# Performance work log

Measured on AMD Instinct MI355X. Metric: run time of the kernel, lower is better.

The kernel has to match this reference:

```python
import jax, jax.numpy as jnp
import numpy as np

H, W = 256, 256
DX, DY = 1.0, 1.0
EI, KC, GC = 1.0, 1.0, 1.0
LAYERS = [2, 256, 512, 1024, H * W]
B = 64


def _d2x(f, dx):
    # reflect-pad width 1 on x (last axis), stencil [1, -2, 1]
    p = jnp.pad(f, ((0, 0), (0, 0), (0, 0), (1, 1)), mode='reflect')
    return (p[..., :-2] - 2.0 * p[..., 1:-1] + p[..., 2:]) / (dx * dx)


def _d2y(f, dy):
    p = jnp.pad(f, ((0, 0), (0, 0), (1, 1), (0, 0)), mode='reflect')
    return (p[:, :, :-2, :] - 2.0 * p[:, :, 1:-1, :] + p[:, :, 2:, :]) / (dy * dy)


def setup_inputs() -> dict:
    key = jax.random.key(0)
    ks = jax.random.split(key, 10)
    inp = {
        'x_coloc': jax.random.normal(ks[0], (B, LAYERS[0]), jnp.float32),
        'P': jax.random.normal(ks[1], (B, H * W), jnp.float32),
    }
    for i in range(4):
        inp[f'W{i + 1}'] = jax.random.normal(ks[2 + i], (LAYERS[i], LAYERS[i + 1]), jnp.float32) / np.sqrt(LAYERS[i]).astype(np.float32)
        inp[f'b{i + 1}'] = jnp.zeros((LAYERS[i + 1],), jnp.float32)
    return inp


def reference(x_coloc, P, W1, b1, W2, b2, W3, b3, W4, b4):
    # MLP field predictor: Linear+ReLU x3, final Linear -> [B, H*W]
    h = jax.nn.relu(x_coloc @ W1 + b1)
    h = jax.nn.relu(h @ W2 + b2)
    h = jax.nn.relu(h @ W3 + b3)
    f = h @ W4 + b4                      # [B, H*W]
    fm = f.reshape(B, 1, H, W)

    fx2 = _d2x(fm, DX)                   # d2/dx2
    fy2 = _d2y(fm, DY)                   # d2/dy2
    lap = fx2 + fy2
    biharmonic = _d2x(lap, DX) + _d2y(lap, DY)

    residual = EI * biharmonic + GC * (fx2 + fy2) + KC * fm - P.reshape(B, 1, H, W)
    return residual.reshape(B, H * W)
```

## Files before the change

kernel.cpp:

```cpp
#include <hip/hip_runtime.h>
#include <hip/hip_bf16.h>


#define BATCH 64
#define NPIX 65536

typedef __attribute__((ext_vector_type(8))) short short8_t;
typedef __attribute__((ext_vector_type(4))) float f32x4;

__device__ __forceinline__ short f2bf(float x) {
    __hip_bfloat16 h = __float2bfloat16(x);
    short s;
    __builtin_memcpy(&s, &h, 2);
    return s;
}

__global__ void k_layer12(const float* __restrict__ x, const float* __restrict__ W1,
                          const float* __restrict__ b1, const float* __restrict__ W2,
                          const float* __restrict__ b2, short* __restrict__ h2b) {
    __shared__ float As[16][64];
    __shared__ float Ws[64][16];
    int tid = threadIdx.x;
    int tn = tid & 15, tm = tid >> 4;
    int n0 = blockIdx.x * 16, m0 = blockIdx.y * 16;
    float acc = 0.f;
    for (int k0 = 0; k0 < 256; k0 += 64) {
#pragma unroll
        for (int j = 0; j < 4; ++j) {
            int e = j * 256 + tid;
            int m = m0 + (e >> 6), kk = k0 + (e & 63);
            float v = x[m * 2 + 0] * W1[kk] + x[m * 2 + 1] * W1[256 + kk] + b1[kk];
            As[e >> 6][e & 63] = v > 0.f ? v : 0.f;
        }
#pragma unroll
        for (int j = 0; j < 4; ++j) {
            int e = j * 256 + tid;
            Ws[e >> 4][e & 15] = W2[(k0 + (e >> 4)) * 512 + n0 + (e & 15)];
        }
        __syncthreads();
#pragma unroll
        for (int k = 0; k < 64; ++k)
            acc += As[tm][k] * Ws[k][tn];
        __syncthreads();
    }
    acc += b2[n0 + tn];
    acc = acc > 0.f ? acc : 0.f;
    h2b[(m0 + tm) * 512 + n0 + tn] = f2bf(acc);
}

__global__ __launch_bounds__(64) void k_layer3(
        const short* __restrict__ A,
        const float* __restrict__ W3,
        const float* __restrict__ b3,
        short* __restrict__ h3b) {
    __shared__ float Wt[2][32 * 16];
    const int lane = threadIdx.x;
    const int lr = lane & 15;
    const int g = lane >> 4;
    const int n0 = blockIdx.x * 16;

    f32x4 acc[4];
#pragma unroll
    for (int a = 0; a < 4; ++a) acc[a] = {0.f, 0.f, 0.f, 0.f};

    const short* ap = A + lr * 512 + g * 8;

    auto stage = [&](int b, int s) {
#pragma unroll
        for (int i = 0; i < 2; ++i) {
            int c = i * 64 + lane;
            int k = c >> 2, q = c & 3;
            const float* src = W3 + (size_t)(s * 32 + k) * 1024 + n0 + q * 4;
            __builtin_amdgcn_global_load_lds(
                (const __attribute__((address_space(1))) void*)src,
                (__attribute__((address_space(3))) void*)((char*)&Wt[b][0] + c * 16),
                16, 0, 0);
        }
    };

    short8_t aC[4], aN[4];
    stage(0, 0);
#pragma unroll
    for (int mt = 0; mt < 4; ++mt)
        aC[mt] = *(const short8_t*)(ap + mt * 8192);

    for (int s = 0; s < 16; ++s) {
        const int cur = s & 1;
        if (s < 15) {
            stage(cur ^ 1, s + 1);
#pragma unroll
            for (int mt = 0; mt < 4; ++mt)
                aN[mt] = *(const short8_t*)(ap + mt * 8192 + (s + 1) * 32);
            asm volatile("s_waitcnt vmcnt(6)" ::: "memory");
        } else {
            asm volatile("s_waitcnt vmcnt(0)" ::: "memory");
        }
        __builtin_amdgcn_sched_barrier(0);

        short8_t bfr;
#pragma unroll
        for (int j = 0; j < 8; ++j)
            bfr[j] = f2bf(Wt[cur][(g * 8 + j) * 16 + lr]);
#pragma unroll
        for (int mt = 0; mt < 4; ++mt)
            acc[mt] = __builtin_amdgcn_mfma_f32_16x16x32_bf16(aC[mt], bfr, acc[mt], 0, 0, 0);

        if (s < 15) {
#pragma unroll
            for (int mt = 0; mt < 4; ++mt) aC[mt] = aN[mt];
        }
    }

    float bb = b3[n0 + lr];
#pragma unroll
    for (int mt = 0; mt < 4; ++mt) {
        int rowb = mt * 16 + g * 4;
#pragma unroll
        for (int r = 0; r < 4; ++r) {
            float v = acc[mt][r] + bb;
            v = v > 0.f ? v : 0.f;
            h3b[(rowb + r) * 1024 + n0 + lr] = f2bf(v);
        }
    }
}

__global__ __launch_bounds__(256) void k_gemm_mfma(
        const short* __restrict__ A,
        const float* __restrict__ W,
        const float* __restrict__ bias,
        float* __restrict__ f) {
    __shared__ float Wt[2][32 * 128];
    __shared__ short At[2][4 * 64 * 8];
    const int tid = threadIdx.x;
    const int w = tid >> 6;
    const int lane = tid & 63;
    const int lr = lane & 15;
    const int g = lane >> 4;
    const int n0 = blockIdx.x * 128;

    f32x4 acc[4][2];
#pragma unroll
    for (int a = 0; a < 4; ++a)
#pragma unroll
        for (int b = 0; b < 2; ++b)
            acc[a][b] = {0.f, 0.f, 0.f, 0.f};

    auto stage = [&](int b, int s) {
#pragma unroll
        for (int i = 0; i < 4; ++i) {
            int c = i * 256 + tid;
            int k = c >> 5;
            int q4 = (c & 31) * 4;
            int csw = q4 ^ (((k >> 3) & 1) << 4);
            const float* src = W + (size_t)(s * 32 + k) * NPIX + n0 + csw;
            __builtin_amdgcn_global_load_lds(
                (const __attribute__((address_space(1))) void*)src,
                (__attribute__((address_space(3))) void*)((char*)&Wt[b][0] + c * 16),
                16, 0, 0);
        }
        {
            int kq = tid >> 6;
            int ms = tid & 63;
            int md = ms ^ (kq << 2);
            const short* asrc = A + md * 1024 + s * 32 + kq * 8;
            __builtin_amdgcn_global_load_lds(
                (const __attribute__((address_space(1))) void*)asrc,
                (__attribute__((address_space(3))) void*)((char*)&At[b][0] + tid * 16),
                16, 0, 0);
        }
    };

    stage(0, 0);

    for (int s = 0; s < 32; ++s) {
        const int cur = s & 1;
        if (s < 31) {
            stage(cur ^ 1, s + 1);
            asm volatile("s_waitcnt vmcnt(5)" ::: "memory");
        } else {
            asm volatile("s_waitcnt vmcnt(0)" ::: "memory");
        }
        __builtin_amdgcn_sched_barrier(0);
        __builtin_amdgcn_s_barrier();
        __builtin_amdgcn_sched_barrier(0);

        short8_t afr[4];
#pragma unroll
        for (int mt = 0; mt < 4; ++mt) {
            int mrow = mt * 16 + lr;
            afr[mt] = *(const short8_t*)((const short*)&At[cur][0] +
                                         g * 512 + (mrow ^ (g << 2)) * 8);
        }
#pragma unroll
        for (int t = 0; t < 2; ++t) {
            const int col = w * 32 + t * 16 + lr;
            const int csw = col ^ ((g & 1) << 4);
            short8_t bfr;
#pragma unroll
            for (int j = 0; j < 8; ++j)
                bfr[j] = f2bf(Wt[cur][(g * 8 + j) * 128 + csw]);
#pragma unroll
            for (int mt = 0; mt < 4; ++mt)
                acc[mt][t] = __builtin_amdgcn_mfma_f32_16x16x32_bf16(afr[mt], bfr, acc[mt][t], 0, 0, 0);
        }
        __builtin_amdgcn_s_barrier();
    }

    __syncthreads();
    float* Cl = (float*)&Wt[0][0];
#pragma unroll
    for (int t = 0; t < 2; ++t) {
        const int colb = w * 32 + t * 16 + lr;
        float bb = bias[n0 + colb];
#pragma unroll
        for (int mt = 0; mt < 4; ++mt)
#pragma unroll
            for (int r = 0; r < 4; ++r)
                Cl[(mt * 16 + g * 4 + r) * 128 + colb] = acc[mt][t][r] + bb;
    }
    __syncthreads();
#pragma unroll
    for (int it = 0; it < 8; ++it) {
        int row = (tid >> 5) + it * 8;
        int cc = (tid & 31) * 4;
        f32x4 v = *(const f32x4*)&Cl[row * 128 + cc];
        *(f32x4*)(f + (size_t)row * NPIX + n0 + cc) = v;
    }
}

#define ROWS 16
__device__ __forceinline__ int rfl(int i) {
    return i < 0 ? -i : (i > 255 ? 510 - i : i);
}
__global__ void k_stencil(const float* __restrict__ f, const float* __restrict__ P,
                          float* __restrict__ out) {
    __shared__ float fs[ROWS + 4][256];
    __shared__ float ls[ROWS + 2][256];
    int x = threadIdx.x;
    int y0 = blockIdx.x * ROWS;
    int b = blockIdx.y;
    const float* fb = f + (size_t)b * NPIX;
#pragma unroll
    for (int t = 0; t < ROWS + 4; ++t) {
        int gy = rfl(y0 - 2 + t);
        fs[t][x] = fb[gy * 256 + x];
    }
    __syncthreads();

    int xm = x == 0 ? 1 : x - 1;
    int xp = x == 255 ? 254 : x + 1;

#pragma unroll
    for (int t = 0; t < ROWS + 2; ++t) {
        int jj = rfl(y0 - 1 + t);
        int s  = jj - y0 + 2;
        int sm = rfl(jj - 1) - y0 + 2;
        int sp = rfl(jj + 1) - y0 + 2;
        float c = fs[s][x];
        ls[t][x] = (fs[sm][x] - 2.f * c + fs[sp][x]) +
                   (fs[s][xm] - 2.f * c + fs[s][xp]);
    }
    __syncthreads();

#pragma unroll
    for (int r = 0; r < ROWS; ++r) {
        int y = y0 + r;
        float lc = ls[r + 1][x];
        float bih = (ls[r][x] - 2.f * lc + ls[r + 2][x]) +
                    (ls[r + 1][xm] - 2.f * lc + ls[r + 1][xp]);
        float fc = fs[r + 2][x];
        size_t idx = (size_t)b * NPIX + y * 256 + x;
        out[idx] = bih + lc + fc - P[idx];
    }
}

extern "C" void kernel_launch(void* const* d_in, const int* in_sizes, int n_in,
                              void* d_out, int out_size, void* d_ws, size_t ws_size,
                              hipStream_t stream) {
    const float* x  = (const float*)d_in[0];
    const float* P  = (const float*)d_in[1];
    const float* W1 = (const float*)d_in[2];
    const float* b1 = (const float*)d_in[3];
    const float* W2 = (const float*)d_in[4];
    const float* b2 = (const float*)d_in[5];
    const float* W3 = (const float*)d_in[6];
    const float* b3 = (const float*)d_in[7];
    const float* W4 = (const float*)d_in[8];
    const float* b4 = (const float*)d_in[9];
    float* out = (float*)d_out;

    char* ws = (char*)d_ws;
    short* h2b = (short*)(ws);
    short* h3b = (short*)(ws + (128 << 10));
    float* f   = (float*)(ws + (256 << 10));

    k_layer12<<<dim3(512 / 16, 4), 256, 0, stream>>>(x, W1, b1, W2, b2, h2b);
    k_layer3<<<64, 64, 0, stream>>>(h2b, W3, b3, h3b);
    k_gemm_mfma<<<NPIX / 128, 256, 0, stream>>>(h3b, W4, b4, f);
    k_stencil<<<dim3(256 / ROWS, BATCH), 256, 0, stream>>>(f, P, out);
}
```

Baseline: 77.95 us.

## Rewrite layer1-2 kernel with bf16 MFMA and async LDS double-buffered W2 loads

Replaces the scalar fp32 shared-memory GEMM for layers 1-2 with a single-wave kernel that computes layer-1 activations in registers, converts them to bf16 and feeds MFMA 16x16x32 instructions. W2 tiles are streamed into LDS with global_load_lds in a double-buffered pipeline. This aims to cut the small-GEMM latency at the cost of bf16 rounding of layer-1 activations and W2, and fewer blocks (32 single-wave blocks).

```diff
diff --git a/kernel.cpp b/kernel.cpp
--- a/kernel.cpp
+++ b/kernel.cpp
@@ -15,37 +15,95 @@
     return s;
 }
 
-__global__ void k_layer12(const float* __restrict__ x, const float* __restrict__ W1,
-                          const float* __restrict__ b1, const float* __restrict__ W2,
-                          const float* __restrict__ b2, short* __restrict__ h2b) {
-    __shared__ float As[16][64];
-    __shared__ float Ws[64][16];
-    int tid = threadIdx.x;
-    int tn = tid & 15, tm = tid >> 4;
-    int n0 = blockIdx.x * 16, m0 = blockIdx.y * 16;
-    float acc = 0.f;
-    for (int k0 = 0; k0 < 256; k0 += 64) {
-#pragma unroll
-        for (int j = 0; j < 4; ++j) {
-            int e = j * 256 + tid;
-            int m = m0 + (e >> 6), kk = k0 + (e & 63);
-            float v = x[m * 2 + 0] * W1[kk] + x[m * 2 + 1] * W1[256 + kk] + b1[kk];
-            As[e >> 6][e & 63] = v > 0.f ? v : 0.f;
-        }
-#pragma unroll
-        for (int j = 0; j < 4; ++j) {
-            int e = j * 256 + tid;
-            Ws[e >> 4][e & 15] = W2[(k0 + (e >> 4)) * 512 + n0 + (e & 15)];
-        }
-        __syncthreads();
-#pragma unroll
-        for (int k = 0; k < 64; ++k)
-            acc += As[tm][k] * Ws[k][tn];
-        __syncthreads();
-    }
-    acc += b2[n0 + tn];
-    acc = acc > 0.f ? acc : 0.f;
-    h2b[(m0 + tm) * 512 + n0 + tn] = f2bf(acc);
+__global__ __launch_bounds__(64) void k_layer12(
+        const float* __restrict__ x,
+        const float* __restrict__ W1,
+        const float* __restrict__ b1,
+        const float* __restrict__ W2,
+        const float* __restrict__ b2,
+        short* __restrict__ h2b) {
+    __shared__ float Wt[2][32 * 16];
+    const int lane = threadIdx.x;
+    const int lr = lane & 15;
+    const int g = lane >> 4;
+    const int n0 = blockIdx.x * 16;
+
+    f32x4 acc[4];
+#pragma unroll
+    for (int a = 0; a < 4; ++a) acc[a] = {0.f, 0.f, 0.f, 0.f};
+
+    float x0[4], x1[4];
+#pragma unroll
+    for (int mt = 0; mt < 4; ++mt) {
+        x0[mt] = x[(mt * 16 + lr) * 2 + 0];
+        x1[mt] = x[(mt * 16 + lr) * 2 + 1];
+    }
+    f32x4 w0v[16], w1v[16], bv[16];
+#pragma unroll
+    for (int i = 0; i < 16; ++i) {
+        int kb = (i >> 1) * 32 + g * 8 + (i & 1) * 4;
+        w0v[i] = *(const f32x4*)(W1 + kb);
+        w1v[i] = *(const f32x4*)(W1 + 256 + kb);
+        bv[i]  = *(const f32x4*)(b1 + kb);
+    }
+
+    auto stage = [&](int b, int s) {
+#pragma unroll
+        for (int i = 0; i < 2; ++i) {
+            int c = i * 64 + lane;
+            int k = c >> 2, q = c & 3;
+            const float* src = W2 + (size_t)(s * 32 + k) * 512 + n0 + q * 4;
+            __builtin_amdgcn_global_load_lds(
+                (const __attribute__((address_space(1))) void*)src,
+                (__attribute__((address_space(3))) void*)((char*)&Wt[b][0] + c * 16),
+                16, 0, 0);
+        }
+    };
+
+    stage(0, 0);
+
+#pragma unroll
+    for (int s = 0; s < 8; ++s) {
+        const int cur = s & 1;
+        if (s < 7) {
+            stage(cur ^ 1, s + 1);
+            asm volatile("s_waitcnt vmcnt(2)" ::: "memory");
+        } else {
+            asm volatile("s_waitcnt vmcnt(0)" ::: "memory");
+        }
+        __builtin_amdgcn_sched_barrier(0);
+
+        short8_t afr[4];
+#pragma unroll
+        for (int mt = 0; mt < 4; ++mt)
+#pragma unroll
+            for (int j = 0; j < 8; ++j) {
+                float v = x0[mt] * w0v[s * 2 + (j >> 2)][j & 3]
+                        + x1[mt] * w1v[s * 2 + (j >> 2)][j & 3]
+                        + bv[s * 2 + (j >> 2)][j & 3];
+                afr[mt][j] = f2bf(v > 0.f ? v : 0.f);
+            }
+
+        short8_t bfr;
+#pragma unroll
+        for (int j = 0; j < 8; ++j)
+            bfr[j] = f2bf(Wt[cur][(g * 8 + j) * 16 + lr]);
+#pragma unroll
+        for (int mt = 0; mt < 4; ++mt)
+            acc[mt] = __builtin_amdgcn_mfma_f32_16x16x32_bf16(afr[mt], bfr, acc[mt], 0, 0, 0);
+    }
+
+    float bb = b2[n0 + lr];
+#pragma unroll
+    for (int mt = 0; mt < 4; ++mt) {
+        int rowb = mt * 16 + g * 4;
+#pragma unroll
+        for (int r = 0; r < 4; ++r) {
+            float v = acc[mt][r] + bb;
+            v = v > 0.f ? v : 0.f;
+            h2b[(rowb + r) * 512 + n0 + lr] = f2bf(v);
+        }
+    }
 }
 
 __global__ __launch_bounds__(64) void k_layer3(
@@ -294,7 +352,7 @@
     short* h3b = (short*)(ws + (128 << 10));
     float* f   = (float*)(ws + (256 << 10));
 
-    k_layer12<<<dim3(512 / 16, 4), 256, 0, stream>>>(x, W1, b1, W2, b2, h2b);
+    k_layer12<<<512 / 16, 64, 0, stream>>>(x, W1, b1, W2, b2, h2b);
     k_layer3<<<64, 64, 0, stream>>>(h2b, W3, b3, h3b);
     k_gemm_mfma<<<NPIX / 128, 256, 0, stream>>>(h3b, W4, b4, f);
     k_stencil<<<dim3(256 / ROWS, BATCH), 256, 0, stream>>>(f, P, out);
```

After: 77.18 us (median of 2 runs). Within noise of the previous version (-1.0%).
